# Kernel tuning notes

Measured on AMD Instinct MI355X. Metric: run time of the kernel, lower is better.

Reference implementation:

```python
import jax, jax.numpy as jnp
import numpy as np

N, C, TX, TY = 32, 256, 1024, 1024


def setup_inputs() -> dict:
    key = jax.random.key(0)
    ks = jax.random.split(key, 9)
    s = 1.0 / np.sqrt(C)
    return {
        "Q": jax.random.normal(ks[0], (N, C, TY), dtype=jnp.float32),
        "K": jax.random.normal(ks[1], (N, C, TX), dtype=jnp.float32),
        "V": jax.random.normal(ks[2], (N, C, TX), dtype=jnp.float32),
        "Wq": jax.random.normal(ks[3], (C, C), dtype=jnp.float32) * s,
        "bq": jax.random.normal(ks[4], (C,), dtype=jnp.float32) * 0.01,
        "Wk": jax.random.normal(ks[5], (C, C), dtype=jnp.float32) * s,
        "bk": jax.random.normal(ks[6], (C,), dtype=jnp.float32) * 0.01,
        "Wv": jax.random.normal(ks[7], (C, C), dtype=jnp.float32) * s,
        "bv": jax.random.normal(ks[8], (C,), dtype=jnp.float32) * 0.01,
    }


def _proj_tanh(W, b, x):
    # 1x1 conv over channels: (C_out, C_in) x (N, C_in, T) -> (N, C_out, T)
    return jnp.tanh(jnp.einsum("oc,nct->not", W, x) + b[None, :, None])


def reference(Q, K, V, Wq, bq, Wk, bk, Wv, bv):
    d_k = Q.shape[1]
    Qp = _proj_tanh(Wq, bq, Q)  # (N, C, Ty)
    Kp = _proj_tanh(Wk, bk, K)  # (N, C, Tx)
    Vp = _proj_tanh(Wv, bv, V)  # (N, C, Tx)
    scores = jnp.einsum("ncs,nct->nst", Kp, Qp) / jnp.sqrt(
        jnp.asarray(d_k, dtype=Q.dtype)
    )  # (N, Tx, Ty)
    A = jax.nn.softmax(scores, axis=1)  # softmax over Tx (dim=1)
    R = jnp.einsum("ncs,nst->nct", Vp, A)  # (N, C, Ty)
    return (R, A)
```

## Files before the change

kernel.cpp:

```cpp
#include <hip/hip_runtime.h>
#include <stdint.h>

#define N_B 32
#define C_D 256
#define T_D 1024

typedef unsigned short u16;
typedef __attribute__((ext_vector_type(8))) short short8;
typedef __attribute__((ext_vector_type(4))) float f32x4;

__device__ __forceinline__ u16 f2bf(float f) {
    unsigned x = __float_as_uint(f);
    return (u16)((x + 0x7fffu + ((x >> 16) & 1u)) >> 16);
}

__device__ __forceinline__ void gld16(const void* g, void* l) {
    __builtin_amdgcn_global_load_lds(
        (const __attribute__((address_space(1))) uint32_t*)g,
        (__attribute__((address_space(3))) uint32_t*)l, 16, 0, 0);
}

__global__ __launch_bounds__(256) void ct_f2b(const float* __restrict__ X,
                                              u16* __restrict__ XT) {
    __shared__ u16 lds[64][65];
    const int n  = blockIdx.z;
    const int t0 = blockIdx.x * 64;
    const int c0 = blockIdx.y * 64;
    const float* Xn = X + (size_t)n * (C_D * T_D);
    u16* XTn = XT + (size_t)n * (T_D * C_D);
    const int tid = threadIdx.x;
    const int row = tid >> 2;
    const int tq  = (tid & 3) * 16;
    const float* src = Xn + (size_t)(c0 + row) * T_D + t0 + tq;
#pragma unroll
    for (int i = 0; i < 4; ++i) {
        float4 v = *(const float4*)(src + i * 4);
        lds[row][tq + i * 4 + 0] = f2bf(v.x);
        lds[row][tq + i * 4 + 1] = f2bf(v.y);
        lds[row][tq + i * 4 + 2] = f2bf(v.z);
        lds[row][tq + i * 4 + 3] = f2bf(v.w);
    }
    __syncthreads();
    const int r  = tid >> 3;
    const int c8 = (tid & 7) * 8;
#pragma unroll
    for (int p = 0; p < 2; ++p) {
        const int tt = r + p * 32;
        union { u16 u[8]; uint4 v; } o;
#pragma unroll
        for (int j = 0; j < 8; ++j) o.u[j] = lds[c8 + j][tt];
        *(uint4*)(XTn + (size_t)(t0 + tt) * C_D + c0 + c8) = o.v;
    }
}

__global__ __launch_bounds__(256) void conv_f2b(const float* __restrict__ in,
                                                u16* __restrict__ out, int n) {
    int i = blockIdx.x * 256 + threadIdx.x;
    if (i < n) out[i] = f2bf(in[i]);
}

template <int EPI, bool F32OUT>
__global__ __launch_bounds__(256) void gemm_abt(
        const u16* __restrict__ A, const u16* __restrict__ B,
        const float* __restrict__ bias, void* __restrict__ OutV,
        int Kdim, int ldo, long sA, long sB, long sO, float scale)
{
    __shared__ __align__(16) u16 smA[128 * 32];
    __shared__ __align__(16) u16 smB[128 * 32];

    const int nb = blockIdx.z;
    const int n0 = blockIdx.x * 128;
    const int m0 = blockIdx.y * 128;
    const int tid = threadIdx.x;

    const u16* Ab = A + (size_t)nb * sA;
    const u16* Bb = B + (size_t)nb * sB;

    const int srow = tid >> 2;
    const int sk8  = (tid & 3) * 8;
    const u16* gA0 = Ab + (size_t)(m0 + srow) * Kdim + sk8;
    const u16* gA1 = gA0 + (size_t)64 * Kdim;
    const u16* gB0 = Bb + (size_t)(n0 + srow) * Kdim + sk8;
    const u16* gB1 = gB0 + (size_t)64 * Kdim;
    u16* lA0 = smA + tid * 8;
    u16* lA1 = smA + 2048 + tid * 8;
    u16* lB0 = smB + tid * 8;
    u16* lB1 = smB + 2048 + tid * 8;

    const int lane = tid & 63;
    const int w    = tid >> 6;
    const int wm   = (w >> 1) * 64;
    const int wn   = (w & 1) * 64;
    const int l15  = lane & 15;
    const int quad = lane >> 4;

    f32x4 acc[4][4];
#pragma unroll
    for (int i = 0; i < 4; ++i)
#pragma unroll
        for (int j = 0; j < 4; ++j) acc[i][j] = (f32x4){0.f, 0.f, 0.f, 0.f};

    for (int kb = 0; kb < Kdim; kb += 32) {
        gld16(gA0 + kb, lA0);
        gld16(gA1 + kb, lA1);
        gld16(gB0 + kb, lB0);
        gld16(gB1 + kb, lB1);
        __syncthreads();
        short8 af[4], bfr[4];
#pragma unroll
        for (int i = 0; i < 4; ++i) {
            af[i]  = *(const short8*)(smA + (wm + i * 16 + l15) * 32 + quad * 8);
            bfr[i] = *(const short8*)(smB + (wn + i * 16 + l15) * 32 + quad * 8);
        }
#pragma unroll
        for (int mi = 0; mi < 4; ++mi)
#pragma unroll
            for (int ni = 0; ni < 4; ++ni)
                acc[mi][ni] = __builtin_amdgcn_mfma_f32_16x16x32_bf16(
                        af[mi], bfr[ni], acc[mi][ni], 0, 0, 0);
        __syncthreads();
    }

#pragma unroll
    for (int mi = 0; mi < 4; ++mi) {
        const int mb = m0 + wm + mi * 16 + quad * 4;
#pragma unroll
        for (int r = 0; r < 4; ++r) {
            const int m = mb + r;
            float bm = 0.f;
            if (EPI == 2) bm = bias[m];
#pragma unroll
            for (int ni = 0; ni < 4; ++ni) {
                const int nn = n0 + wn + ni * 16 + l15;
                float v = acc[mi][ni][r] * scale;
                if (EPI == 1) v = tanhf(v + bias[nn]);
                if (EPI == 2) v = tanhf(v + bm);
                if (F32OUT)
                    ((float*)OutV)[(size_t)nb * sO + (size_t)m * ldo + nn] = v;
                else
                    ((u16*)OutV)[(size_t)nb * sO + (size_t)m * ldo + nn] = f2bf(v);
            }
        }
    }
}

__global__ __launch_bounds__(256) void softmax_cols(float* __restrict__ S) {
    __shared__ float pm[16][64];
    __shared__ float pl[16][64];
    __shared__ float fM[64];
    __shared__ float fR[64];
    const int n   = blockIdx.y;
    const int t0  = blockIdx.x * 64;
    const int tid = threadIdx.x;
    const int g   = tid >> 4;
    const int ci  = (tid & 15) * 4;
    float* A = S + (size_t)n * T_D * T_D + t0 + ci;
    float* p = A + (size_t)g * 64 * T_D;

    float m[4] = {-1e30f, -1e30f, -1e30f, -1e30f};
    float l[4] = {0.f, 0.f, 0.f, 0.f};
#pragma unroll 8
    for (int s = 0; s < 64; ++s) {
        float4 v = *(const float4*)(p + (size_t)s * T_D);
        float x[4] = {v.x, v.y, v.z, v.w};
#pragma unroll
        for (int j = 0; j < 4; ++j) {
            float nm = fmaxf(m[j], x[j]);
            l[j] = l[j] * __expf(m[j] - nm) + __expf(x[j] - nm);
            m[j] = nm;
        }
    }
#pragma unroll
    for (int j = 0; j < 4; ++j) { pm[g][ci + j] = m[j]; pl[g][ci + j] = l[j]; }
    __syncthreads();
    if (tid < 64) {
        float M = -1e30f;
#pragma unroll
        for (int g2 = 0; g2 < 16; ++g2) M = fmaxf(M, pm[g2][tid]);
        float L = 0.f;
#pragma unroll
        for (int g2 = 0; g2 < 16; ++g2) L += pl[g2][tid] * __expf(pm[g2][tid] - M);
        fM[tid] = M;
        fR[tid] = 1.0f / L;
    }
    __syncthreads();
    float M[4], R[4];
#pragma unroll
    for (int j = 0; j < 4; ++j) { M[j] = fM[ci + j]; R[j] = fR[ci + j]; }
#pragma unroll 8
    for (int s = 0; s < 64; ++s) {
        float4 v = *(const float4*)(p + (size_t)s * T_D);
        v.x = __expf(v.x - M[0]) * R[0];
        v.y = __expf(v.y - M[1]) * R[1];
        v.z = __expf(v.z - M[2]) * R[2];
        v.w = __expf(v.w - M[3]) * R[3];
        *(float4*)(p + (size_t)s * T_D) = v;
    }
}

__global__ __launch_bounds__(256) void gemm_r(
        const u16* __restrict__ Vp, const float* __restrict__ S,
        float* __restrict__ R)
{
    __shared__ __align__(16) u16 smA[128 * 32];
    __shared__ __align__(16) u16 smB[128 * 32];

    const int nb = blockIdx.z;
    const int n0 = blockIdx.x * 128;
    const int m0 = blockIdx.y * 128;
    const int tid = threadIdx.x;

    const u16* Ab = Vp + (size_t)nb * (C_D * T_D);
    const float* Sb = S + (size_t)nb * T_D * T_D;
    float* Rb = R + (size_t)nb * (C_D * T_D);

    const int srow = tid >> 2;
    const int sk8  = (tid & 3) * 8;
    const u16* gA0 = Ab + (size_t)(m0 + srow) * T_D + sk8;
    const u16* gA1 = gA0 + (size_t)64 * T_D;
    u16* lA0 = smA + tid * 8;
    u16* lA1 = smA + 2048 + tid * 8;

    const int sr = tid >> 3;
    const int tq = (tid & 7) * 16;

    const int lane = tid & 63;
    const int w    = tid >> 6;
    const int wm   = (w >> 1) * 64;
    const int wn   = (w & 1) * 64;
    const int l15  = lane & 15;
    const int quad = lane >> 4;

    f32x4 acc[4][4];
#pragma unroll
    for (int i = 0; i < 4; ++i)
#pragma unroll
        for (int j = 0; j < 4; ++j) acc[i][j] = (f32x4){0.f, 0.f, 0.f, 0.f};

    for (int kb = 0; kb < T_D; kb += 32) {
        gld16(gA0 + kb, lA0);
        gld16(gA1 + kb, lA1);
        const float* srcB = Sb + (size_t)(kb + sr) * T_D + n0 + tq;
#pragma unroll
        for (int i = 0; i < 4; ++i) {
            float4 v = *(const float4*)(srcB + i * 4);
            smB[(tq + i * 4 + 0) * 32 + sr] = f2bf(v.x);
            smB[(tq + i * 4 + 1) * 32 + sr] = f2bf(v.y);
            smB[(tq + i * 4 + 2) * 32 + sr] = f2bf(v.z);
            smB[(tq + i * 4 + 3) * 32 + sr] = f2bf(v.w);
        }
        __syncthreads();
        short8 af[4], bfr[4];
#pragma unroll
        for (int i = 0; i < 4; ++i) {
            af[i]  = *(const short8*)(smA + (wm + i * 16 + l15) * 32 + quad * 8);
            bfr[i] = *(const short8*)(smB + (wn + i * 16 + l15) * 32 + quad * 8);
        }
#pragma unroll
        for (int mi = 0; mi < 4; ++mi)
#pragma unroll
            for (int ni = 0; ni < 4; ++ni)
                acc[mi][ni] = __builtin_amdgcn_mfma_f32_16x16x32_bf16(
                        af[mi], bfr[ni], acc[mi][ni], 0, 0, 0);
        __syncthreads();
    }

#pragma unroll
    for (int mi = 0; mi < 4; ++mi) {
        const int mb = m0 + wm + mi * 16 + quad * 4;
#pragma unroll
        for (int r = 0; r < 4; ++r) {
            const int m = mb + r;
#pragma unroll
            for (int ni = 0; ni < 4; ++ni) {
                const int nn = n0 + wn + ni * 16 + l15;
                Rb[(size_t)m * T_D + nn] = acc[mi][ni][r];
            }
        }
    }
}

extern "C" void kernel_launch(void* const* d_in, const int* in_sizes, int n_in,
                              void* d_out, int out_size, void* d_ws, size_t ws_size,
                              hipStream_t stream) {
    const float* Qf = (const float*)d_in[0];
    const float* Kf = (const float*)d_in[1];
    const float* Vf = (const float*)d_in[2];
    const float* Wq = (const float*)d_in[3];
    const float* bq = (const float*)d_in[4];
    const float* Wk = (const float*)d_in[5];
    const float* bk = (const float*)d_in[6];
    const float* Wv = (const float*)d_in[7];
    const float* bv = (const float*)d_in[8];

    float* Rout = (float*)d_out;
    float* Aout = Rout + (size_t)N_B * C_D * T_D;

    u16* QT  = (u16*)Rout;
    u16* KT  = (u16*)Rout + 8388608;
    u16* VT  = (u16*)Aout;
    u16* Wqb = (u16*)Aout + 8388608;
    u16* Wkb = Wqb + 65536;
    u16* Wvb = Wkb + 65536;
    u16* QpT = (u16*)d_in[0];
    u16* KpT = (u16*)d_in[1];
    u16* Vp  = (u16*)d_in[2];

    dim3 blk(256);
    const long sX = (long)T_D * C_D;
    const long sS = (long)T_D * T_D;

    ct_f2b<<<dim3(16, 4, N_B), blk, 0, stream>>>(Qf, QT);
    ct_f2b<<<dim3(16, 4, N_B), blk, 0, stream>>>(Kf, KT);
    ct_f2b<<<dim3(16, 4, N_B), blk, 0, stream>>>(Vf, VT);
    conv_f2b<<<dim3(256), blk, 0, stream>>>(Wq, Wqb, 65536);
    conv_f2b<<<dim3(256), blk, 0, stream>>>(Wk, Wkb, 65536);
    conv_f2b<<<dim3(256), blk, 0, stream>>>(Wv, Wvb, 65536);

    gemm_abt<1, false><<<dim3(2, 8, N_B), blk, 0, stream>>>(QT, Wqb, bq, QpT, C_D, C_D, sX, 0, sX, 1.0f);
    gemm_abt<1, false><<<dim3(2, 8, N_B), blk, 0, stream>>>(KT, Wkb, bk, KpT, C_D, C_D, sX, 0, sX, 1.0f);
    gemm_abt<2, false><<<dim3(8, 2, N_B), blk, 0, stream>>>(Wvb, VT, bv, Vp, C_D, T_D, 0, sX, sX, 1.0f);

    gemm_abt<0, true><<<dim3(8, 8, N_B), blk, 0, stream>>>(KpT, QpT, nullptr, Aout, C_D, T_D, sX, sX, sS, 0.0625f);

    softmax_cols<<<dim3(16, N_B), blk, 0, stream>>>(Aout);

    gemm_r<<<dim3(8, 2, N_B), blk, 0, stream>>>(Vp, Aout, Rout);
}
```

Measured before the change: 461.0 us.

## Fuse fp32 transpose-convert into GEMM staging with swizzled LDS layout

Drops the separate transpose/bf16-conversion kernels for Q, K, V and instead converts and transposes fp32 inputs directly while staging tiles into LDS inside a templated GEMM. The LDS layout for transposed operands uses an XOR swizzle to reduce bank conflicts, and the final A·V GEMM reuses the same template. Weight conversions are merged into a single launch. This removes a full extra memory pass over the inputs and several launches, at the cost of register-based staging instead of direct global-to-LDS loads.

```diff
diff --git a/kernel.cpp b/kernel.cpp
--- a/kernel.cpp
+++ b/kernel.cpp
@@ -20,48 +20,41 @@
         (__attribute__((address_space(3))) uint32_t*)l, 16, 0, 0);
 }
 
-__global__ __launch_bounds__(256) void ct_f2b(const float* __restrict__ X,
-                                              u16* __restrict__ XT) {
-    __shared__ u16 lds[64][65];
-    const int n  = blockIdx.z;
-    const int t0 = blockIdx.x * 64;
-    const int c0 = blockIdx.y * 64;
-    const float* Xn = X + (size_t)n * (C_D * T_D);
-    u16* XTn = XT + (size_t)n * (T_D * C_D);
-    const int tid = threadIdx.x;
-    const int row = tid >> 2;
-    const int tq  = (tid & 3) * 16;
-    const float* src = Xn + (size_t)(c0 + row) * T_D + t0 + tq;
-#pragma unroll
-    for (int i = 0; i < 4; ++i) {
-        float4 v = *(const float4*)(src + i * 4);
-        lds[row][tq + i * 4 + 0] = f2bf(v.x);
-        lds[row][tq + i * 4 + 1] = f2bf(v.y);
-        lds[row][tq + i * 4 + 2] = f2bf(v.z);
-        lds[row][tq + i * 4 + 3] = f2bf(v.w);
-    }
-    __syncthreads();
-    const int r  = tid >> 3;
-    const int c8 = (tid & 7) * 8;
-#pragma unroll
-    for (int p = 0; p < 2; ++p) {
-        const int tt = r + p * 32;
-        union { u16 u[8]; uint4 v; } o;
-#pragma unroll
-        for (int j = 0; j < 8; ++j) o.u[j] = lds[c8 + j][tt];
-        *(uint4*)(XTn + (size_t)(t0 + tt) * C_D + c0 + c8) = o.v;
-    }
-}
-
-__global__ __launch_bounds__(256) void conv_f2b(const float* __restrict__ in,
-                                                u16* __restrict__ out, int n) {
+__global__ __launch_bounds__(256) void conv_w(const float* __restrict__ w0,
+                                              const float* __restrict__ w1,
+                                              const float* __restrict__ w2,
+                                              u16* __restrict__ o0,
+                                              u16* __restrict__ o1,
+                                              u16* __restrict__ o2) {
+    const float* in = blockIdx.y == 0 ? w0 : (blockIdx.y == 1 ? w1 : w2);
+    u16* out       = blockIdx.y == 0 ? o0 : (blockIdx.y == 1 ? o1 : o2);
     int i = blockIdx.x * 256 + threadIdx.x;
-    if (i < n) out[i] = f2bf(in[i]);
-}
-
-template <int EPI, bool F32OUT>
-__global__ __launch_bounds__(256) void gemm_abt(
-        const u16* __restrict__ A, const u16* __restrict__ B,
+    out[i] = f2bf(in[i]);
+}
+
+__device__ __forceinline__ void stage_tr(const float* __restrict__ src,
+                                         u16* __restrict__ sm, int tid) {
+    const int sr2 = tid >> 4;
+    const int tt8 = (tid & 15) * 8;
+    float4 v0 = *(const float4*)(src);
+    float4 v1 = *(const float4*)(src + 4);
+    float4 w0 = *(const float4*)(src + T_D);
+    float4 w1 = *(const float4*)(src + T_D + 4);
+    float a[8] = {v0.x, v0.y, v0.z, v0.w, v1.x, v1.y, v1.z, v1.w};
+    float b[8] = {w0.x, w0.y, w0.z, w0.w, w1.x, w1.y, w1.z, w1.w};
+    const int kk = sr2 * 2;
+#pragma unroll
+    for (int j = 0; j < 8; ++j) {
+        const int t  = tt8 + j;
+        const int ks = kk ^ (((t >> 4) & 3) << 3);
+        uint32_t pk = (uint32_t)f2bf(a[j]) | ((uint32_t)f2bf(b[j]) << 16);
+        *(uint32_t*)(sm + t * 32 + ks) = pk;
+    }
+}
+
+template <bool TRA, bool TRB, int EPI, bool F32OUT>
+__global__ __launch_bounds__(256) void gemm_t(
+        const void* __restrict__ Av, const void* __restrict__ Bv,
         const float* __restrict__ bias, void* __restrict__ OutV,
         int Kdim, int ldo, long sA, long sB, long sO, float scale)
 {
@@ -73,19 +66,31 @@
     const int m0 = blockIdx.y * 128;
     const int tid = threadIdx.x;
 
-    const u16* Ab = A + (size_t)nb * sA;
-    const u16* Bb = B + (size_t)nb * sB;
-
     const int srow = tid >> 2;
     const int sk8  = (tid & 3) * 8;
-    const u16* gA0 = Ab + (size_t)(m0 + srow) * Kdim + sk8;
-    const u16* gA1 = gA0 + (size_t)64 * Kdim;
-    const u16* gB0 = Bb + (size_t)(n0 + srow) * Kdim + sk8;
-    const u16* gB1 = gB0 + (size_t)64 * Kdim;
-    u16* lA0 = smA + tid * 8;
-    u16* lA1 = smA + 2048 + tid * 8;
-    u16* lB0 = smB + tid * 8;
-    u16* lB1 = smB + 2048 + tid * 8;
+    const int sr2  = tid >> 4;
+    const int tt8  = (tid & 15) * 8;
+
+    const u16* gA0 = nullptr; const u16* gA1 = nullptr;
+    const float* tA = nullptr;
+    if constexpr (TRA) {
+        tA = (const float*)Av + (size_t)nb * sA + (size_t)(sr2 * 2) * T_D + m0 + tt8;
+    } else {
+        const u16* Ab = (const u16*)Av + (size_t)nb * sA;
+        gA0 = Ab + (size_t)(m0 + srow) * Kdim + sk8;
+        gA1 = gA0 + (size_t)64 * Kdim;
+    }
+    const u16* gB0 = nullptr; const u16* gB1 = nullptr;
+    const float* tB = nullptr;
+    if constexpr (TRB) {
+        tB = (const float*)Bv + (size_t)nb * sB + (size_t)(sr2 * 2) * T_D + n0 + tt8;
+    } else {
+        const u16* Bb = (const u16*)Bv + (size_t)nb * sB;
+        gB0 = Bb + (size_t)(n0 + srow) * Kdim + sk8;
+        gB1 = gB0 + (size_t)64 * Kdim;
+    }
+    u16* lA0 = smA + tid * 8; u16* lA1 = smA + 2048 + tid * 8;
+    u16* lB0 = smB + tid * 8; u16* lB1 = smB + 2048 + tid * 8;
 
     const int lane = tid & 63;
     const int w    = tid >> 6;
@@ -101,16 +106,28 @@
         for (int j = 0; j < 4; ++j) acc[i][j] = (f32x4){0.f, 0.f, 0.f, 0.f};
 
     for (int kb = 0; kb < Kdim; kb += 32) {
-        gld16(gA0 + kb, lA0);
-        gld16(gA1 + kb, lA1);
-        gld16(gB0 + kb, lB0);
-        gld16(gB1 + kb, lB1);
+        if constexpr (TRA) {
+            stage_tr(tA + (size_t)kb * T_D, smA, tid);
+        } else {
+            gld16(gA0 + kb, lA0);
+            gld16(gA1 + kb, lA1);
+        }
+        if constexpr (TRB) {
+            stage_tr(tB + (size_t)kb * T_D, smB, tid);
+        } else {
+            gld16(gB0 + kb, lB0);
+            gld16(gB1 + kb, lB1);
+        }
         __syncthreads();
         short8 af[4], bfr[4];
 #pragma unroll
         for (int i = 0; i < 4; ++i) {
-            af[i]  = *(const short8*)(smA + (wm + i * 16 + l15) * 32 + quad * 8);
-            bfr[i] = *(const short8*)(smB + (wn + i * 16 + l15) * 32 + quad * 8);
+            const int ra = wm + i * 16 + l15;
+            const int ca = TRA ? ((quad ^ ((ra >> 4) & 3)) * 8) : (quad * 8);
+            af[i] = *(const short8*)(smA + ra * 32 + ca);
+            const int rb = wn + i * 16 + l15;
+            const int cb = TRB ? ((quad ^ ((rb >> 4) & 3)) * 8) : (quad * 8);
+            bfr[i] = *(const short8*)(smB + rb * 32 + cb);
         }
 #pragma unroll
         for (int mi = 0; mi < 4; ++mi)
@@ -198,88 +215,6 @@
     }
 }
 
-__global__ __launch_bounds__(256) void gemm_r(
-        const u16* __restrict__ Vp, const float* __restrict__ S,
-        float* __restrict__ R)
-{
-    __shared__ __align__(16) u16 smA[128 * 32];
-    __shared__ __align__(16) u16 smB[128 * 32];
-
-    const int nb = blockIdx.z;
-    const int n0 = blockIdx.x * 128;
-    const int m0 = blockIdx.y * 128;
-    const int tid = threadIdx.x;
-
-    const u16* Ab = Vp + (size_t)nb * (C_D * T_D);
-    const float* Sb = S + (size_t)nb * T_D * T_D;
-    float* Rb = R + (size_t)nb * (C_D * T_D);
-
-    const int srow = tid >> 2;
-    const int sk8  = (tid & 3) * 8;
-    const u16* gA0 = Ab + (size_t)(m0 + srow) * T_D + sk8;
-    const u16* gA1 = gA0 + (size_t)64 * T_D;
-    u16* lA0 = smA + tid * 8;
-    u16* lA1 = smA + 2048 + tid * 8;
-
-    const int sr = tid >> 3;
-    const int tq = (tid & 7) * 16;
-
-    const int lane = tid & 63;
-    const int w    = tid >> 6;
-    const int wm   = (w >> 1) * 64;
-    const int wn   = (w & 1) * 64;
-    const int l15  = lane & 15;
-    const int quad = lane >> 4;
-
-    f32x4 acc[4][4];
-#pragma unroll
-    for (int i = 0; i < 4; ++i)
-#pragma unroll
-        for (int j = 0; j < 4; ++j) acc[i][j] = (f32x4){0.f, 0.f, 0.f, 0.f};
-
-    for (int kb = 0; kb < T_D; kb += 32) {
-        gld16(gA0 + kb, lA0);
-        gld16(gA1 + kb, lA1);
-        const float* srcB = Sb + (size_t)(kb + sr) * T_D + n0 + tq;
-#pragma unroll
-        for (int i = 0; i < 4; ++i) {
-            float4 v = *(const float4*)(srcB + i * 4);
-            smB[(tq + i * 4 + 0) * 32 + sr] = f2bf(v.x);
-            smB[(tq + i * 4 + 1) * 32 + sr] = f2bf(v.y);
-            smB[(tq + i * 4 + 2) * 32 + sr] = f2bf(v.z);
-            smB[(tq + i * 4 + 3) * 32 + sr] = f2bf(v.w);
-        }
-        __syncthreads();
-        short8 af[4], bfr[4];
-#pragma unroll
-        for (int i = 0; i < 4; ++i) {
-            af[i]  = *(const short8*)(smA + (wm + i * 16 + l15) * 32 + quad * 8);
-            bfr[i] = *(const short8*)(smB + (wn + i * 16 + l15) * 32 + quad * 8);
-        }
-#pragma unroll
-        for (int mi = 0; mi < 4; ++mi)
-#pragma unroll
-            for (int ni = 0; ni < 4; ++ni)
-                acc[mi][ni] = __builtin_amdgcn_mfma_f32_16x16x32_bf16(
-                        af[mi], bfr[ni], acc[mi][ni], 0, 0, 0);
-        __syncthreads();
-    }
-
-#pragma unroll
-    for (int mi = 0; mi < 4; ++mi) {
-        const int mb = m0 + wm + mi * 16 + quad * 4;
-#pragma unroll
-        for (int r = 0; r < 4; ++r) {
-            const int m = mb + r;
-#pragma unroll
-            for (int ni = 0; ni < 4; ++ni) {
-                const int nn = n0 + wn + ni * 16 + l15;
-                Rb[(size_t)m * T_D + nn] = acc[mi][ni][r];
-            }
-        }
-    }
-}
-
 extern "C" void kernel_launch(void* const* d_in, const int* in_sizes, int n_in,
                               void* d_out, int out_size, void* d_ws, size_t ws_size,
                               hipStream_t stream) {
@@ -296,34 +231,31 @@
     float* Rout = (float*)d_out;
     float* Aout = Rout + (size_t)N_B * C_D * T_D;
 
-    u16* QT  = (u16*)Rout;
-    u16* KT  = (u16*)Rout + 8388608;
-    u16* VT  = (u16*)Aout;
-    u16* Wqb = (u16*)Aout + 8388608;
+    u16* QpT = (u16*)Rout;
+    u16* KpT = (u16*)Rout + 8388608;
+    u16* Wqb = (u16*)Aout;
     u16* Wkb = Wqb + 65536;
     u16* Wvb = Wkb + 65536;
-    u16* QpT = (u16*)d_in[0];
-    u16* KpT = (u16*)d_in[1];
-    u16* Vp  = (u16*)d_in[2];
+    u16* Vp  = (u16*)d_in[0];
 
     dim3 blk(256);
-    const long sX = (long)T_D * C_D;
+    const long sX = (long)C_D * T_D;
     const long sS = (long)T_D * T_D;
 
-    ct_f2b<<<dim3(16, 4, N_B), blk, 0, stream>>>(Qf, QT);
-    ct_f2b<<<dim3(16, 4, N_B), blk, 0, stream>>>(Kf, KT);
-    ct_f2b<<<dim3(16, 4, N_B), blk, 0, stream>>>(Vf, VT);
-    conv_f2b<<<dim3(256), blk, 0, stream>>>(Wq, Wqb, 65536);
-    conv_f2b<<<dim3(256), blk, 0, stream>>>(Wk, Wkb, 65536);
-    conv_f2b<<<dim3(256), blk, 0, stream>>>(Wv, Wvb, 65536);
-
-    gemm_abt<1, false><<<dim3(2, 8, N_B), blk, 0, stream>>>(QT, Wqb, bq, QpT, C_D, C_D, sX, 0, sX, 1.0f);
-    gemm_abt<1, false><<<dim3(2, 8, N_B), blk, 0, stream>>>(KT, Wkb, bk, KpT, C_D, C_D, sX, 0, sX, 1.0f);
-    gemm_abt<2, false><<<dim3(8, 2, N_B), blk, 0, stream>>>(Wvb, VT, bv, Vp, C_D, T_D, 0, sX, sX, 1.0f);
-
-    gemm_abt<0, true><<<dim3(8, 8, N_B), blk, 0, stream>>>(KpT, QpT, nullptr, Aout, C_D, T_D, sX, sX, sS, 0.0625f);
+    conv_w<<<dim3(256, 3), blk, 0, stream>>>(Wq, Wk, Wv, Wqb, Wkb, Wvb);
+
+    gemm_t<true, false, 1, false><<<dim3(2, 8, N_B), blk, 0, stream>>>(
+            Qf, Wqb, bq, QpT, C_D, C_D, sX, 0, sX, 1.0f);
+    gemm_t<true, false, 1, false><<<dim3(2, 8, N_B), blk, 0, stream>>>(
+            Kf, Wkb, bk, KpT, C_D, C_D, sX, 0, sX, 1.0f);
+    gemm_t<false, true, 2, false><<<dim3(8, 2, N_B), blk, 0, stream>>>(
+            Wvb, Vf, bv, Vp, C_D, T_D, 0, sX, sX, 1.0f);
+
+    gemm_t<false, false, 0, true><<<dim3(8, 8, N_B), blk, 0, stream>>>(
+            KpT, QpT, nullptr, Aout, C_D, T_D, sX, sX, sS, 0.0625f);
 
     softmax_cols<<<dim3(16, N_B), blk, 0, stream>>>(Aout);
 
-    gemm_r<<<dim3(8, 2, N_B), blk, 0, stream>>>(Vp, Aout, Rout);
-}
+    gemm_t<false, true, 0, true><<<dim3(8, 2, N_B), blk, 0, stream>>>(
+            Vp, Aout, nullptr, Rout, T_D, T_D, sX, sS, sX, 1.0f);
+}
```

Result: faster. 418.8 us (-9.2%).
